# Optimization experiments

Measured on AMD Instinct MI355X. Metric: run time of the kernel, lower is better.

## Reference

```python
import math
import jax, jax.numpy as jnp
from jax import lax
import numpy as np

C = 256; A = 3; NIMG = 2; L = 5
SIZES = [(200, 304), (100, 152), (50, 76), (25, 38), (13, 19)]
STRIDES = [4, 8, 16, 32, 64]
LVTOP = 600          # cfg['lvtop'] (eval)
IMTOP = 300          # cfg['imtop1'] (eval)
SCORE_THR = 0.0      # cfg['score_thr1']
MIN_SIZE = 1e-2      # cfg['min_size1']
IOU_THR = 0.7        # cfg['iou_thr1']
IMH, IMW = 800.0, 1216.0
BBOX_CLIP = math.log(1000.0 / 16.0)   # clamp=True in decode_boxes
GROUP_OFF = 4096.0                     # > max canvas coord -> disjoint NMS groups


def _level_anchors(h, w, stride):
    scale = stride * 8.0
    r = np.array([0.5, 1.0, 2.0])
    ws = scale * np.sqrt(r); hs = scale / np.sqrt(r)          # [A]
    ys, xs = np.meshgrid(np.arange(h), np.arange(w), indexing='ij')
    cx = (xs.reshape(-1, 1) + 0.5) * stride                    # [HW,1]
    cy = (ys.reshape(-1, 1) + 0.5) * stride
    a = np.stack([cx - ws / 2, cy - hs / 2, cx + ws / 2, cy + hs / 2], axis=-1)
    return a.reshape(-1, 4).astype(np.float32)                 # [HW*A,4]


def setup_inputs() -> dict:
    key = jax.random.key(0)
    ks = jax.random.split(key, 10)
    inp = {}
    for i, (h, w) in enumerate(SIZES):
        inp[f'fmap{i}'] = jax.random.normal(ks[i], (NIMG, C, h, w), jnp.float32)
        inp[f'priors{i}'] = jnp.asarray(_level_anchors(h, w, STRIDES[i]))
    inp['imsizes'] = jnp.array([[IMH, IMW]] * NIMG, jnp.float32)   # (h, w) per image
    inp['conv_w'] = jax.random.normal(ks[5], (C, C, 3, 3), jnp.float32) * 0.03
    inp['conv_b'] = jnp.zeros((C,), jnp.float32)
    inp['log_w'] = jax.random.normal(ks[6], (A, C), jnp.float32) * 0.03
    inp['log_b'] = jnp.zeros((A,), jnp.float32)
    inp['reg_w'] = jax.random.normal(ks[7], (A * 4, C), jnp.float32) * 0.01
    inp['reg_b'] = jnp.zeros((A * 4,), jnp.float32)
    return inp


def _decode(reg, pri):
    pw = pri[..., 2] - pri[..., 0]; ph = pri[..., 3] - pri[..., 1]
    pcx = pri[..., 0] + 0.5 * pw;   pcy = pri[..., 1] + 0.5 * ph
    dx, dy = reg[..., 0], reg[..., 1]
    dw = jnp.minimum(reg[..., 2], BBOX_CLIP)
    dh = jnp.minimum(reg[..., 3], BBOX_CLIP)
    cx = dx * pw + pcx; cy = dy * ph + pcy
    w = pw * jnp.exp(dw); h = ph * jnp.exp(dh)
    return jnp.stack([cx - 0.5 * w, cy - 0.5 * h, cx + 0.5 * w, cy + 0.5 * h], axis=-1)


def _forward(fmaps, priors, imsizes, conv_w, conv_b, log_w, log_b, reg_w, reg_b):
    dn = ('NCHW', 'OIHW', 'NCHW')
    boxes_l, score_l = [], []
    for x, pri in zip(fmaps, priors):
        n = x.shape[0]
        h = jax.nn.relu(lax.conv_general_dilated(x, conv_w, (1, 1), 'SAME',
                                                 dimension_numbers=dn)
                        + conv_b[None, :, None, None])
        logit = (jnp.einsum('nchw,ac->nahw', h, log_w)
                 + log_b[None, :, None, None]).transpose(0, 2, 3, 1).reshape(n, -1)
        reg = (jnp.einsum('nchw,ac->nahw', h, reg_w)
               + reg_b[None, :, None, None]).transpose(0, 2, 3, 1).reshape(n, -1, 4)
        vals, top = lax.top_k(logit, LVTOP)                        # per-level topk
        reg_g = jnp.take_along_axis(reg, jnp.broadcast_to(top[:, :, None], (n, LVTOP, 4)), axis=1)
        pri_g = pri[top]                                           # [n,k,4]
        boxes_l.append(_decode(reg_g, pri_g))
        score_l.append(jax.nn.sigmoid(vals))
    boxes = jnp.concatenate(boxes_l, axis=1)                       # [n, L*k, 4]
    obj = jnp.concatenate(score_l, axis=1)                         # [n, L*k]
    n, dim = boxes.shape[0], boxes.shape[1]
    Nall = n * dim
    boxes = boxes.reshape(Nall, 4); obj = obj.reshape(Nall)
    imidx = jnp.arange(Nall) // dim
    lvl = jnp.tile(jnp.repeat(jnp.arange(L), LVTOP), n)
    valid = obj >= SCORE_THR
    sz = imsizes[imidx]                                            # [Nall,2] (h,w)
    boxes = jnp.stack([jnp.clip(boxes[:, 0], 0.0, sz[:, 1]),
                       jnp.clip(boxes[:, 1], 0.0, sz[:, 0]),
                       jnp.clip(boxes[:, 2], 0.0, sz[:, 1]),
                       jnp.clip(boxes[:, 3], 0.0, sz[:, 0])], axis=-1)
    valid = valid & (boxes[:, 2] - boxes[:, 0] >= MIN_SIZE) & (boxes[:, 3] - boxes[:, 1] >= MIN_SIZE)
    groups = imidx * 10 + lvl                                      # batched_nms groups
    # sort by score, invalid entries pushed to the end
    order = jnp.argsort(-jnp.where(valid, obj, -1.0))
    b = boxes[order]; v = valid[order]; g = groups[order]; im = imidx[order]
    # group-offset trick == torchvision batched_nms
    ob = b + g.astype(b.dtype)[:, None] * GROUP_OFF
    area = (ob[:, 2] - ob[:, 0]) * (ob[:, 3] - ob[:, 1])
    lt = jnp.maximum(ob[:, None, :2], ob[None, :, :2])
    rb = jnp.minimum(ob[:, None, 2:], ob[None, :, 2:])
    wh = jnp.maximum(rb - lt, 0.0)
    inter = wh[..., 0] * wh[..., 1]
    iou = lax.stop_gradient(inter / (area[:, None] + area[None, :] - inter))
    idxr = jnp.arange(Nall)
    def body(i, keep):
        sup = jnp.any(keep & (iou[i] > IOU_THR) & (idxr < i))
        return keep.at[i].set(v[i] & ~sup)
    keep = lax.fori_loop(0, Nall, body, jnp.zeros((Nall,), bool))
    # per-image cap at IMTOP (keep is already in score order)
    sel = keep[None, :] & (im[None, :] == jnp.arange(n)[:, None])  # [n,Nall]
    sel = sel & (jnp.cumsum(sel, axis=1) <= IMTOP)
    prio = jnp.where(sel, Nall - idxr[None, :], 0)
    pvals, pos = lax.top_k(prio, IMTOP)                            # [n,IMTOP]
    vout = pvals > 0
    bout = jnp.where(vout[..., None], b[pos], 0.0)                 # [n,IMTOP,4]
    imout = jnp.broadcast_to(jnp.arange(n)[:, None], (n, IMTOP)).reshape(-1).astype(jnp.int32)
    return bout.reshape(-1, 4), imout, vout.reshape(-1)


def reference(fmap0, fmap1, fmap2, fmap3, fmap4,
              priors0, priors1, priors2, priors3, priors4,
              imsizes, conv_w, conv_b, log_w, log_b, reg_w, reg_b):
    return _forward([fmap0, fmap1, fmap2, fmap3, fmap4],
                    [priors0, priors1, priors2, priors3, priors4],
                    imsizes, conv_w, conv_b, log_w, log_b, reg_w, reg_b)
```

## Files before the change

### kernel.cpp

```cpp
#include <hip/hip_runtime.h>
#include <math.h>

typedef unsigned long long u64;
typedef unsigned int u32;
typedef unsigned short u16;
typedef _Float16 f16;
typedef __attribute__((ext_vector_type(8))) _Float16 f16x8;
typedef __attribute__((ext_vector_type(8))) unsigned short ushort8;
typedef __attribute__((ext_vector_type(4))) float f32x4;

#define LVTOP 600
#define IMTOP 300
#define NIMG 2
#define NLVL 5
#define NCAND (NLVL*LVTOP)

__constant__ int d_HW[5]    = {60800,15200,3800,950,247};
__constant__ int d_LGOFF[5] = {0,364800,456000,478800,484500};
__constant__ int d_RGOFF[5] = {0,1459200,1824000,1915200,1938000};
__constant__ int d_H[5]  = {200,100,50,25,13};
__constant__ int d_W[5]  = {304,152,76,38,19};
__constant__ int d_TX[5] = {7,4,2,1,1};
__constant__ long d_XB[5] = {0, 31129600, 38912000, 40857600, 41344000};
__constant__ long d_CB[5] = {0, 3891200, 4864000, 5107200, 5168000};
#define NCHUNK 5183808
#define NXB 20250
#define WS_NEED 178889200ull

__device__ __forceinline__ u32 okey(float f){
  u32 u = __float_as_uint(f);
  return (u & 0x80000000u) ? ~u : (u | 0x80000000u);
}

__device__ __forceinline__ void f16_split(float v, u16& hb, u16& lb){
  f16 h = (f16)v;
  float r = v - (float)h;
  f16 l = (f16)r;
  hb = __builtin_bit_cast(u16, h);
  lb = __builtin_bit_cast(u16, l);
}

__device__ __forceinline__ u64 shfl64(u64 v, int src){
  u32 lo = __shfl((u32)v, src);
  u32 hi = __shfl((u32)(v >> 32), src);
  return ((u64)hi << 32) | lo;
}

__device__ __forceinline__ void dma16(const u16* g, u16* l){
  __builtin_amdgcn_global_load_lds(
      (const __attribute__((address_space(1))) u32*)g,
      (__attribute__((address_space(3))) u32*)l, 16, 0, 0);
}

template<int NN, int NT>
__device__ void bitonic_desc64(u64* a, int tid){
  for (int k = 2; k <= NN; k <<= 1){
    for (int j = k >> 1; j > 0; j >>= 1){
      __syncthreads();
      for (int i = tid; i < NN; i += NT){
        int ixj = i ^ j;
        if (ixj > i){
          u64 x = a[i], y = a[ixj];
          bool up = ((i & k) == 0);
          if (up ? (x < y) : (x > y)){ a[i] = y; a[ixj] = x; }
        }
      }
    }
  }
  __syncthreads();
}

template<int NN, int NT>
__device__ void bitonic_asc32(u32* a, int tid){
  for (int k = 2; k <= NN; k <<= 1){
    for (int j = k >> 1; j > 0; j >>= 1){
      __syncthreads();
      for (int i = tid; i < NN; i += NT){
        int ixj = i ^ j;
        if (ixj > i){
          u32 x = a[i], y = a[ixj];
          bool up = ((i & k) == 0);
          if (up ? (x > y) : (x < y)){ a[i] = y; a[ixj] = x; }
        }
      }
    }
  }
  __syncthreads();
}

__device__ void suffix_scan(u32* s, int NB, int tid){
  for (int off = 1; off < NB; off <<= 1){
    u32 v0 = 0, v1 = 0;
    int i1 = tid + 1024;
    if (tid < NB) v0 = s[tid] + ((tid + off < NB) ? s[tid + off] : 0u);
    if (i1  < NB) v1 = s[i1]  + ((i1  + off < NB) ? s[i1  + off] : 0u);
    __syncthreads();
    if (tid < NB) s[tid] = v0;
    if (i1  < NB) s[i1]  = v1;
    __syncthreads();
  }
}

__global__ __launch_bounds__(256) void prep(
    const float* __restrict__ f0, const float* __restrict__ f1,
    const float* __restrict__ f2, const float* __restrict__ f3,
    const float* __restrict__ f4,
    u16* __restrict__ xh, u16* __restrict__ xl, u16* __restrict__ zp,
    const float* __restrict__ cw, const float* __restrict__ lw,
    const float* __restrict__ rw, u16* __restrict__ wT, u16* __restrict__ whB,
    u32* __restrict__ ghist, int xsb)
{
  int t = threadIdx.x;
  if ((int)blockIdx.x >= xsb){
    int bid = blockIdx.x - xsb;
    if (bid < 72){
      int id = bid*256 + t;
      int cc = id & 7;
      int co = (id >> 3) & 255;
      int tap = id >> 11;
      int ntg = co >> 4;
      size_t base = (size_t)((tap*8 + cc)*16 + ntg) * 1024;
      #pragma unroll
      for (int ci = 0; ci < 32; ci++){
        float v = cw[(size_t)co*2304 + (size_t)(cc*32 + ci)*9 + tap];
        u16 hi, lo; f16_split(v, hi, lo);
        int q = ci >> 3, j = ci & 7;
        int lane = q*16 + (co & 15);
        wT[base + lane*8 + j] = hi;
        wT[base + 512 + lane*8 + j] = lo;
      }
    } else if (bid == 72){
      if (t < 128){
        int ks = t >> 4, nn = t & 15;
        for (int ci = 0; ci < 32; ci++){
          int k = ks*32 + ci;
          float v = 0.0f;
          if (nn < 3) v = lw[nn*256 + k];
          else if (nn < 15) v = rw[(nn-3)*256 + k];
          u16 hi, lo; f16_split(v, hi, lo);
          int q = ci >> 3, j = ci & 7;
          int lane = q*16 + nn;
          whB[ks*1024 + lane*8 + j] = hi;
          whB[ks*1024 + 512 + lane*8 + j] = lo;
        }
      }
    } else {
      int z = (bid - 73)*1024 + t;
      #pragma unroll
      for (int q = 0; q < 4; q++){
        int i = z + q*256;
        if (i < NLVL*NIMG*2048) ghist[i] = 0;
      }
    }
    return;
  }
  long id = (long)blockIdx.x*256 + t;
  if (blockIdx.x == 0 && t < 8) zp[t] = 0;
  if (id >= NCHUNK) return;
  int l = (id < d_CB[1]) ? 0 : (id < d_CB[2]) ? 1 : (id < d_CB[3]) ? 2 : (id < d_CB[4]) ? 3 : 4;
  long rem = id - d_CB[l];
  int HW = d_HW[l];
  int n = (int)(rem / (32*HW));
  int r2 = (int)(rem - (long)n*32*HW);
  int cg = r2 / HW;
  int p = r2 - cg*HW;
  const float* fm = (l==0)?f0:(l==1)?f1:(l==2)?f2:(l==3)?f3:f4;
  const float* gp = fm + ((size_t)(n*256 + cg*8))*HW + p;
  ushort8 hv, lv;
  #pragma unroll
  for (int j = 0; j < 8; j++){
    float v = gp[(size_t)j*HW];
    u16 hb, lb; f16_split(v, hb, lb);
    hv[j] = hb; lv[j] = lb;
  }
  *(ushort8*)&xh[id*8] = hv;
  *(ushort8*)&xl[id*8] = lv;
}

__global__ __launch_bounds__(256, 2) void conv_mfma(
    const float* __restrict__ f0, const float* __restrict__ f1,
    const float* __restrict__ f2, const float* __restrict__ f3,
    const float* __restrict__ f4,
    const u16* __restrict__ xh, const u16* __restrict__ xl,
    const u16* __restrict__ zp,
    const u16* __restrict__ wT, const u16* __restrict__ whB,
    const float* __restrict__ cb, const float* __restrict__ lb,
    const float* __restrict__ rb,
    float* __restrict__ lgb, float* __restrict__ rgb,
    u32* __restrict__ ghist, int use_dma)
{
  __shared__ __align__(16) u16 smem[26624];

  const int t = threadIdx.x;
  const int n = blockIdx.y;
  int bx = blockIdx.x;
  int l, rbk;
  if (bx < 700){ l = 0; rbk = bx; }
  else if (bx < 900){ l = 1; rbk = bx - 700; }
  else if (bx < 950){ l = 2; rbk = bx - 900; }
  else if (bx < 963){ l = 3; rbk = bx - 950; }
  else { l = 4; rbk = bx - 963; }
  const int H = d_H[l], W = d_W[l], tilesX = d_TX[l];
  const int ty2 = rbk / tilesX;
  const int x0 = (rbk - ty2*tilesX) * 48;
  const float* fm = (l==0) ? f0 : (l==1) ? f1 : (l==2) ? f2 : (l==3) ? f3 : f4;

  const int wave = t >> 6, lane = t & 63;
  const int quad = lane >> 4, l15 = lane & 15;
  const int HWp = H * W;
  const float* xin = fm + (size_t)n * 256 * HWp;

  f32x4 acc[2][3][4];
  #pragma unroll
  for (int r = 0; r < 2; r++)
    #pragma unroll
    for (int a = 0; a < 3; a++)
      #pragma unroll
      for (int b = 0; b < 4; b++) acc[r][a][b] = (f32x4){0.f,0.f,0.f,0.f};

  auto compute_cc = [&](int cc, int bufo){
    #pragma unroll
    for (int ky = 0; ky < 3; ky++){
      #pragma unroll
      for (int kx = 0; kx < 3; kx++){
        const u16* bt = wT + (size_t)((((ky*3+kx)*8 + cc)*16) + wave*4) * 1024 + lane*8;
        f16x8 Bh[4], Bl[4];
        #pragma unroll
        for (int nt = 0; nt < 4; nt++){
          Bh[nt] = *(const f16x8*)(bt + nt*1024);
// ... 94 lines not shown
  for (int i = t; i < 2048; i += 256) lhist[i] = 0;

  u16* hA_h = smem;
  u16* hA_l = smem + 8704;
  #pragma unroll
  for (int row = 0; row < 2; row++){
    const int ty = ty2*2 + row;
    const bool rowok = (ty < H);
    if (rowok){
      f32x4 a2 = (f32x4){0.f,0.f,0.f,0.f};
      #pragma unroll
      for (int half = 0; half < 2; half++){
        if ((wave >> 1) == half){
          #pragma unroll
          for (int mt = 0; mt < 3; mt++){
            #pragma unroll
            for (int nt = 0; nt < 4; nt++){
              int col = (wave & 1)*64 + nt*16 + l15;
              float bias = cb[half*128 + col];
              #pragma unroll
              for (int r = 0; r < 4; r++){
                float h = fmaxf(acc[row][mt][nt][r] + bias, 0.0f);
                u16 hb, lb2; f16_split(h, hb, lb2);
                int pos = mt*16 + quad*4 + r;
                hA_h[pos*136 + col] = hb;
                hA_l[pos*136 + col] = lb2;
              }
            }
          }
        }
        __syncthreads();
        #pragma unroll
        for (int ks2 = 0; ks2 < 4; ks2++){
          int ks = half*4 + ks2;
          int ao = (wave*16 + l15)*136 + ks2*32 + quad*8;
          f16x8 Ah = *(const f16x8*)&hA_h[ao];
          f16x8 Al = *(const f16x8*)&hA_l[ao];
          const u16* wb = whB + ks*1024 + lane*8;
          f16x8 Bh = *(const f16x8*)wb;
          f16x8 Bl = *(const f16x8*)(wb + 512);
          a2 = __builtin_amdgcn_mfma_f32_16x16x32_f16(Ah, Bh, a2, 0,0,0);
          a2 = __builtin_amdgcn_mfma_f32_16x16x32_f16(Al, Bh, a2, 0,0,0);
          a2 = __builtin_amdgcn_mfma_f32_16x16x32_f16(Ah, Bl, a2, 0,0,0);
        }
        __syncthreads();
      }

      float* sm_out = (float*)smem;
      {
        int o = l15;
        float bias = (o < 3) ? lb[o] : ((o < 15) ? rb[o-3] : 0.0f);
        #pragma unroll
        for (int r = 0; r < 4; r++){
          int pos = wave*16 + quad*4 + r;
          sm_out[pos*16 + o] = a2[r] + bias;
        }
      }
      __syncthreads();
      {
        int P = W - x0; if (P > 48) P = 48;
        size_t pbase = (size_t)ty * W + x0;
        float* lg = lgb + d_LGOFF[l] + (size_t)n*HWp*3  + pbase*3;
        float* rg = rgb + d_RGOFF[l] + (size_t)n*HWp*12 + pbase*12;
        for (int j = t; j < P*3; j += 256){
          float v = sm_out[(j/3)*16 + (j%3)];
          lg[j] = v;
          atomicAdd(&lhist[okey(v) >> 21], 1u);
        }
        for (int j = t; j < P*12; j += 256) rg[j] = sm_out[(j/12)*16 + 3 + (j%12)];
      }
      __syncthreads();
    }
  }

  {
    u32* gh = ghist + (size_t)(l*NIMG + n) * 2048;
    for (int i = t; i < 2048; i += 256){
      u32 h = lhist[i];
      if (h) atomicAdd(&gh[i], h);
    }
  }
}

__global__ __launch_bounds__(1024) void topk_decode(
    const float* __restrict__ lg, const float* __restrict__ rg,
    const float* __restrict__ pr0, const float* __restrict__ pr1,
    const float* __restrict__ pr2, const float* __restrict__ pr3,
    const float* __restrict__ pr4,
    const float* __restrict__ imsizes, const u32* __restrict__ ghist,
    float* __restrict__ cbox, float* __restrict__ cscore, u32* __restrict__ cvalid)
{
  __shared__ u32 hist[2048];
  __shared__ u32 sscan[2048];
  __shared__ u64 sel[1024];
  __shared__ u32 eqbuf[1024];
  __shared__ u32 scal[8];
  int tid = threadIdx.x;
  int l = blockIdx.x / NIMG;
  int n = blockIdx.x - l*NIMG;
  int HW = d_HW[l];
  int N = HW * 3;
  const float* lgl = lg + d_LGOFF[l] + (size_t)n * N;

  {
    const u32* gh = ghist + (size_t)blockIdx.x * 2048;
    for (int i = tid; i < 2048; i += 1024){ u32 h = gh[i]; hist[i] = h; sscan[i] = h; }
  }
  __syncthreads();
  suffix_scan(sscan, 2048, tid);
  if (tid < 2048){
    u32 Si = sscan[tid], Sn = (tid+1 < 2048) ? sscan[tid+1] : 0u;
    if (Si >= LVTOP && Sn < LVTOP){ scal[0] = (u32)tid; scal[1] = Si - hist[tid]; }
  }
  { int i2 = tid + 1024;
    u32 Si = sscan[i2], Sn = (i2+1 < 2048) ? sscan[i2+1] : 0u;
    if (Si >= LVTOP && Sn < LVTOP){ scal[0] = (u32)i2; scal[1] = Si - hist[i2]; } }
  __syncthreads();
  u32 B1 = scal[0], base1 = scal[1];

  for (int i = tid; i < 2048; i += 1024) hist[i] = 0;
  __syncthreads();
  for (int i = tid; i < N; i += 1024){
    u32 k = okey(lgl[i]);
    if ((k >> 21) == B1) atomicAdd(&hist[(k >> 10) & 0x7FFu], 1u);
  }
  __syncthreads();
  for (int i = tid; i < 2048; i += 1024) sscan[i] = hist[i];
  __syncthreads();
  suffix_scan(sscan, 2048, tid);
  {
    u32 need = LVTOP - base1;
    if (tid < 2048){
      u32 Si = sscan[tid], Sn = (tid+1 < 2048) ? sscan[tid+1] : 0u;
      if (Si >= need && Sn < need){ scal[2] = (u32)tid; scal[3] = base1 + Si - hist[tid]; }
    }
    int i2 = tid + 1024;
    u32 Si = sscan[i2], Sn = (i2+1 < 2048) ? sscan[i2+1] : 0u;
    if (Si >= need && Sn < need){ scal[2] = (u32)i2; scal[3] = base1 + Si - hist[i2]; }
  }
  __syncthreads();
  u32 B2 = scal[2], base2 = scal[3];

  for (int i = tid; i < 1024; i += 1024) hist[i] = 0;
  __syncthreads();
  u32 hi21 = (B1 << 11) | B2;
  for (int i = tid; i < N; i += 1024){
    u32 k = okey(lgl[i]);
    if ((k >> 10) == hi21) atomicAdd(&hist[k & 0x3FFu], 1u);
  }
  __syncthreads();
  for (int i = tid; i < 1024; i += 1024) sscan[i] = hist[i];
  __syncthreads();
  suffix_scan(sscan, 1024, tid);
  {
    u32 need = LVTOP - base2;
    if (tid < 1024){
      u32 Si = sscan[tid], Sn = (tid+1 < 1024) ? sscan[tid+1] : 0u;
      if (Si >= need && Sn < need){
        scal[4] = (hi21 << 10) | (u32)tid;
        scal[5] = base2 + Si - hist[tid];
      }
    }
  }
  if (tid == 0){ scal[6] = 0; scal[7] = 0; }
  __syncthreads();
  u32 T = scal[4], nAbove = scal[5], needEq = LVTOP - scal[5];

  for (int i = tid; i < 1024; i += 1024) sel[i] = 0;
  __syncthreads();
  for (int i = tid; i < N; i += 1024){
    u32 k = okey(lgl[i]);
    if (k > T){
      u32 p = atomicAdd(&scal[6], 1u);
      sel[p] = ((u64)k << 32) | (0xFFFFFFFFu - (u32)i);
    } else if (k == T){
      u32 p = atomicAdd(&scal[7], 1u);
      if (p < 1024) eqbuf[p] = (u32)i;
    }
  }
  __syncthreads();
  u32 cntE = scal[7];
  if (cntE > needEq){
    u32 m = cntE < 1024u ? cntE : 1024u;
    for (int i = tid; i < 1024; i += 1024) if ((u32)i >= m) eqbuf[i] = 0xFFFFFFFFu;
    __syncthreads();
    bitonic_asc32<1024,1024>(eqbuf, tid);
  }
  __syncthreads();
  if ((u32)tid < needEq)
    sel[nAbove + tid] = ((u64)T << 32) | (0xFFFFFFFFu - eqbuf[tid]);
  __syncthreads();
  {
    u64 mykey = sel[tid];
    int rank = 0;
    for (int j = 0; j < 1024; j++) rank += (sel[j] > mykey) ? 1 : 0;
    __syncthreads();
    sel[rank] = mykey;
  }
  __syncthreads();

  if (tid < LVTOP){
    u64 c = sel[tid];
    u32 i = 0xFFFFFFFFu - (u32)c;
    float val = lgl[i];
    float score = 1.0f / (1.0f + expf(-val));
    int pp = (int)i / 3, a = (int)i - pp*3;
    const float* pri;
    if (l == 0) pri = pr0; else if (l == 1) pri = pr1; else if (l == 2) pri = pr2;
    else if (l == 3) pri = pr3; else pri = pr4;
    pri += (size_t)i * 4;
    const float* rgp = rg + d_RGOFF[l] + ((size_t)n * HW + pp) * 12 + a * 4;
    float px0 = pri[0], py0 = pri[1], px1 = pri[2], py1 = pri[3];
    float pw = px1 - px0, ph = py1 - py0;
    float pcx = px0 + 0.5f*pw, pcy = py0 + 0.5f*ph;
    const float BC = (float)4.135166556742356;
    float dx = rgp[0], dy = rgp[1];
    float dw = fminf(rgp[2], BC), dh = fminf(rgp[3], BC);
    float cx = dx*pw + pcx, cy = dy*ph + pcy;
    float bw = pw * expf(dw), bh = ph * expf(dh);
    float x1 = cx - 0.5f*bw, y1 = cy - 0.5f*bh;
    float x2 = cx + 0.5f*bw, y2 = cy + 0.5f*bh;
    float imh = imsizes[n*2+0], imw = imsizes[n*2+1];
    x1 = fminf(fmaxf(x1, 0.0f), imw);
    y1 = fminf(fmaxf(y1, 0.0f), imh);
    x2 = fminf(fmaxf(x2, 0.0f), imw);
    y2 = fminf(fmaxf(y2, 0.0f), imh);
    u32 valid = (score >= 0.0f) && ((x2 - x1) >= 1e-2f) && ((y2 - y1) >= 1e-2f);
    int ci = n*NCAND + l*LVTOP + tid;
    cbox[ci*4+0] = x1; cbox[ci*4+1] = y1; cbox[ci*4+2] = x2; cbox[ci*4+3] = y2;
    cscore[ci] = score; cvalid[ci] = valid;
  }
}

__global__ __launch_bounds__(1024) void sort_cand(
    const float* __restrict__ cscore, const u32* __restrict__ cvalid,
    const float* __restrict__ cbox,
    float* __restrict__ sbox, float* __restrict__ sob,
    float* __restrict__ sarea, u32* __restrict__ svalid,
    u32* __restrict__ rlist, u32* __restrict__ kflag)
{
  __shared__ u64 a[4096];
  int tid = threadIdx.x, n = blockIdx.x;
  for (int i = tid; i < 4096; i += 1024){
    if (i < NCAND){
      int ci = n*NCAND + i;
      float s = cvalid[ci] ? cscore[ci] : -1.0f;
      a[i] = ((u64)okey(s) << 32) | (0xFFFFFFFFu - (u32)i);
    } else a[i] = 0;
  }
  bitonic_desc64<4096,1024>(a, tid);
  int mylvl[3];
  #pragma unroll
  for (int q = 0; q < 3; q++){
    int r = tid + q*1024;
    mylvl[q] = 0;
    if (r < NCAND){
      u32 li = 0xFFFFFFFFu - (u32)a[r];
      int ci = n*NCAND + (int)li;
      float b0 = cbox[ci*4+0], b1 = cbox[ci*4+1], b2 = cbox[ci*4+2], b3 = cbox[ci*4+3];
      int lvl = (int)li / LVTOP;
      mylvl[q] = lvl;
      float off = (float)(n*10 + lvl) * 4096.0f;
      int so = n*NCAND + r;
      sbox[so*4+0]=b0; sbox[so*4+1]=b1; sbox[so*4+2]=b2; sbox[so*4+3]=b3;
      float o0=b0+off, o1=b1+off, o2=b2+off, o3=b3+off;
      sob[so*4+0]=o0; sob[so*4+1]=o1; sob[so*4+2]=o2; sob[so*4+3]=o3;
      sarea[so] = (o2-o0)*(o3-o1);
      svalid[so] = cvalid[ci];
    }
  }
  __syncthreads();
  #pragma unroll
  for (int q = 0; q < 3; q++){
    int r = tid + q*1024;
    a[r] = (r < NCAND) ? (1ull << (12*mylvl[q])) : 0ull;
  }
  a[tid + 3072] = 0ull;
  __syncthreads();
  for (int off = 1; off < 4096; off <<= 1){
    u64 v[4];
    #pragma unroll
    for (int q = 0; q < 4; q++){
      int i = tid + q*1024;
      v[q] = a[i] + ((i >= off) ? a[i-off] : 0ull);
    }
    __syncthreads();
    #pragma unroll
    for (int q = 0; q < 4; q++) a[tid + q*1024] = v[q];
    __syncthreads();
  }
  #pragma unroll
  for (int q = 0; q < 3; q++){
    int r = tid + q*1024;
    if (r < NCAND){
      int lv = mylvl[q];
      int pos = (int)((a[r] >> (12*lv)) & 0xFFFull) - 1;
      rlist[(n*NLVL + lv)*LVTOP + pos] = (u32)r;
      kflag[n*NCAND + r] = 0u;
    }
  }
}

__global__ __launch_bounds__(256) void nms_l(
    const float* __restrict__ sob, const float* __restrict__ sarea,
    const u32* __restrict__ svalid, const u32* __restrict__ rlist,
    u32* __restrict__ kflag)
{
  __shared__ float bx[LVTOP*5];
  __shared__ u64 pm[LVTOP*10];
  int t = threadIdx.x, nl = blockIdx.x, n = nl / NLVL;
  for (int i = t; i < LVTOP; i += 256){
    int so = n*NCAND + (int)rlist[nl*LVTOP + i];
    bx[i*5+0]=sob[so*4+0]; bx[i*5+1]=sob[so*4+1];
    bx[i*5+2]=sob[so*4+2]; bx[i*5+3]=sob[so*4+3];
    bx[i*5+4]=sarea[so];
  }
  __syncthreads();
  for (int i = t; i < LVTOP; i += 256){
    int so = n*NCAND + (int)rlist[nl*LVTOP + i];
    bool act = svalid[so] != 0;
    float oi0=bx[i*5+0], oi1=bx[i*5+1], oi2=bx[i*5+2], oi3=bx[i*5+3], ai=bx[i*5+4];
    for (int w = 0; w < 10; w++){
      u64 bits = 0;
      if (act){
        int jj0 = (i >= w*64) ? (i - w*64 + 1) : 0;
        int jjend = (LVTOP - w*64 < 64) ? (LVTOP - w*64) : 64;
        for (int jj = jj0; jj < jjend; jj++){
          int j = w*64 + jj;
          float oj0=bx[j*5+0], oj1=bx[j*5+1], oj2=bx[j*5+2], oj3=bx[j*5+3], aj=bx[j*5+4];
          float ltx = fmaxf(oi0, oj0), lty = fmaxf(oi1, oj1);
          float rbx = fminf(oi2, oj2), rby = fminf(oi3, oj3);
          float wx = fmaxf(rbx - ltx, 0.0f), wy = fmaxf(rby - lty, 0.0f);
          float inter = wx * wy;
          float iou = inter / ((ai + aj) - inter);
          if (iou > 0.7f) bits |= (1ull << jj);
        }
      }
      pm[i*10 + w] = bits;
    }
  }
  __syncthreads();
  if (t < 64){
    u64 vw = 0, remv = 0;
    for (int c = 0; c < 10; c++){
      int i = c*64 + t;
      int pred = 0;
      if (i < LVTOP) pred = svalid[n*NCAND + (int)rlist[nl*LVTOP + i]] != 0;
      u64 b = __ballot(pred);
      if (t == c) vw = b;
    }
    for (int w = 0; w < 10; w++){
      u64 act = shfl64(vw, w) & ~shfl64(remv, w);
      while (act){
        int bpos = __builtin_ctzll(act);
        int i = w*64 + bpos;
        if (t == 0) kflag[n*NCAND + (int)rlist[nl*LVTOP + i]] = 1u;
        u64 m = (t < 10) ? pm[i*10 + t] : 0ull;
        u64 mw = pm[i*10 + w];
        remv |= m;
        act &= ~(1ull << bpos);
        act &= ~mw;
      }
    }
  }
}

__global__ __launch_bounds__(1024) void merge_out(
    const u32* __restrict__ kflag, const float* __restrict__ sbox,
    float* __restrict__ out)
{
  __shared__ u32 ps[4096];
  int tid = threadIdx.x, n = blockIdx.x;
  u32 f[4];
  #pragma unroll
  for (int q = 0; q < 4; q++){
    int i = tid + q*1024;
    f[q] = (i < NCAND) ? kflag[n*NCAND + i] : 0u;
    ps[i] = f[q];
  }
  __syncthreads();
  for (int off = 1; off < 4096; off <<= 1){
    u32 v[4];
    #pragma unroll
    for (int q = 0; q < 4; q++){
      int i = tid + q*1024;
      v[q] = ps[i] + ((i >= off) ? ps[i-off] : 0u);
    }
    __syncthreads();
    #pragma unroll
    for (int q = 0; q < 4; q++) ps[tid + q*1024] = v[q];
    __syncthreads();
  }
  #pragma unroll
  for (int q = 0; q < 4; q++){
    int i = tid + q*1024;
    if (i < NCAND && f[q] && ps[i] <= IMTOP){
      int slot = n*IMTOP + (int)ps[i] - 1;
      int so = n*NCAND + i;
      out[slot*4+0] = sbox[so*4+0]; out[slot*4+1] = sbox[so*4+1];
      out[slot*4+2] = sbox[so*4+2]; out[slot*4+3] = sbox[so*4+3];
    }
  }
  u32 kept = ps[NCAND-1]; if (kept > IMTOP) kept = IMTOP;
  for (int j = tid; j < IMTOP; j += 1024){
    int slot = n*IMTOP + j;
    if ((u32)j >= kept){
      out[slot*4+0]=0; out[slot*4+1]=0; out[slot*4+2]=0; out[slot*4+3]=0;
    }
    out[2400 + slot] = (float)n;
    out[3000 + slot] = ((u32)j < kept) ? 1.0f : 0.0f;
  }
}

extern "C" void kernel_launch(void* const* d_in, const int* in_sizes, int n_in,
                              void* d_out, int out_size, void* d_ws, size_t ws_size,
                              hipStream_t stream)
{
  const float* fmap[5]   = {(const float*)d_in[0], (const float*)d_in[2], (const float*)d_in[4],
                            (const float*)d_in[6], (const float*)d_in[8]};
  const float* priors[5] = {(const float*)d_in[1], (const float*)d_in[3], (const float*)d_in[5],
                            (const float*)d_in[7], (const float*)d_in[9]};
  const float* imsz   = (const float*)d_in[10];
  const float* conv_w = (const float*)d_in[11];
  const float* conv_b = (const float*)d_in[12];
  const float* log_w  = (const float*)d_in[13];
  const float* log_b  = (const float*)d_in[14];
  const float* reg_w  = (const float*)d_in[15];
  const float* reg_b  = (const float*)d_in[16];

  char* base = (char*)d_ws;
  float* lg     = (float*)(base + 0);
  float* rg     = (float*)(base + 1943928);
  float* cscore = (float*)(base + 9719640);
  float* cbox   = (float*)(base + 9743640);
  u32*   cvalid = (u32*)  (base + 9839640);
  float* sbox   = (float*)(base + 9863640);
  float* sob    = (float*)(base + 9959640);
  float* sarea  = (float*)(base + 10055640);
  u32*   svalid = (u32*)  (base + 10079640);
  u32*   rlist  = (u32*)  (base + 10103640);
  u32*   kflag  = (u32*)  (base + 10127640);
  u32*   ghist  = (u32*)  (base + 10151648);
  u16*   wT     = (u16*)  (base + 10631648);
  u16*   whB    = (u16*)  (base + 12990944);
  u16*   zp     = (u16*)  (base + 13007328);
  u16*   xh     = (u16*)  (base + 13007344);
  u16*   xl     = (u16*)  (base + 95948272);

  int use_dma = (ws_size >= WS_NEED) ? 1 : 0;
  int xsb = use_dma ? NXB : 0;

  prep<<<xsb + 93, 256, 0, stream>>>(
      fmap[0], fmap[1], fmap[2], fmap[3], fmap[4], xh, xl, zp,
      conv_w, log_w, reg_w, wT, whB, ghist, xsb);

  conv_mfma<<<dim3(970, NIMG), 256, 0, stream>>>(
      fmap[0], fmap[1], fmap[2], fmap[3], fmap[4],
      xh, xl, zp, wT, whB, conv_b, log_b, reg_b, lg, rg, ghist, use_dma);

  topk_decode<<<NLVL*NIMG, 1024, 0, stream>>>(lg, rg,
      priors[0], priors[1], priors[2], priors[3], priors[4],
      imsz, ghist, cbox, cscore, cvalid);
  sort_cand<<<NIMG, 1024, 0, stream>>>(cscore, cvalid, cbox, sbox, sob, sarea,
                                       svalid, rlist, kflag);
  nms_l<<<NIMG*NLVL, 256, 0, stream>>>(sob, sarea, svalid, rlist, kflag);
  merge_out<<<NIMG, 1024, 0, stream>>>(kflag, sbox, (float*)d_out);
}
```

Before: 1.133 ms.

## Fuse post-processing kernels into one persistent kernel with grid barriers

Merges topk_decode, sort_cand, nms_l and merge_out into a single 10-block kernel that separates the stages with an atomic spin grid barrier, reset in prep. This removes three kernel launches and their inter-kernel gaps from the serial tail. It relies on all 10 blocks being co-resident. The NMS stage now runs with 1024 threads per block instead of 256, and idle blocks spin on the barrier during the single-block stages.

```diff
diff --git a/kernel.cpp b/kernel.cpp
--- a/kernel.cpp
+++ b/kernel.cpp
@@ -14,6 +14,7 @@
 #define NIMG 2
 #define NLVL 5
 #define NCAND (NLVL*LVTOP)
+#define FNB (NIMG*NLVL)
 
 __constant__ int d_HW[5]    = {60800,15200,3800,950,247};
 __constant__ int d_LGOFF[5] = {0,364800,456000,478800,484500};
@@ -52,6 +53,17 @@
       (__attribute__((address_space(3))) u32*)l, 16, 0, 0);
 }
 
+__device__ __forceinline__ void gsync(u32* bar, u32 target){
+  __threadfence();
+  __syncthreads();
+  if (threadIdx.x == 0){
+    atomicAdd(bar, 1u);
+    while (atomicAdd(bar, 0u) < target){ }
+  }
+  __syncthreads();
+  __threadfence();
+}
+
 template<int NN, int NT>
 __device__ void bitonic_desc64(u64* a, int tid){
   for (int k = 2; k <= NN; k <<= 1){
@@ -108,7 +120,7 @@
     u16* __restrict__ xh, u16* __restrict__ xl, u16* __restrict__ zp,
     const float* __restrict__ cw, const float* __restrict__ lw,
     const float* __restrict__ rw, u16* __restrict__ wT, u16* __restrict__ whB,
-    u32* __restrict__ ghist, int xsb)
+    u32* __restrict__ ghist, u32* __restrict__ bar, int xsb)
 {
   int t = threadIdx.x;
   if ((int)blockIdx.x >= xsb){
@@ -145,6 +157,7 @@
         }
       }
     } else {
+      if (bid == 73 && t == 0) bar[0] = 0;
       int z = (bid - 73)*1024 + t;
       #pragma unroll
       for (int q = 0; q < 4; q++){
@@ -405,333 +418,332 @@
   }
 }
 
-__global__ __launch_bounds__(1024) void topk_decode(
+__global__ __launch_bounds__(1024) void post(
     const float* __restrict__ lg, const float* __restrict__ rg,
     const float* __restrict__ pr0, const float* __restrict__ pr1,
     const float* __restrict__ pr2, const float* __restrict__ pr3,
     const float* __restrict__ pr4,
     const float* __restrict__ imsizes, const u32* __restrict__ ghist,
-    float* __restrict__ cbox, float* __restrict__ cscore, u32* __restrict__ cvalid)
+    float* __restrict__ cbox, float* __restrict__ cscore, u32* __restrict__ cvalid,
+    float* __restrict__ sbox, float* __restrict__ sob,
+    float* __restrict__ sarea, u32* __restrict__ svalid,
+    u32* __restrict__ rlist, u32* __restrict__ kflag,
+    float* __restrict__ out, u32* __restrict__ bar)
 {
-  __shared__ u32 hist[2048];
-  __shared__ u32 sscan[2048];
-  __shared__ u64 sel[1024];
-  __shared__ u32 eqbuf[1024];
-  __shared__ u32 scal[8];
+  __shared__ __align__(16) char smx[60032];
   int tid = threadIdx.x;
-  int l = blockIdx.x / NIMG;
-  int n = blockIdx.x - l*NIMG;
-  int HW = d_HW[l];
-  int N = HW * 3;
-  const float* lgl = lg + d_LGOFF[l] + (size_t)n * N;
+  int b = blockIdx.x;
 
   {
-    const u32* gh = ghist + (size_t)blockIdx.x * 2048;
-    for (int i = tid; i < 2048; i += 1024){ u32 h = gh[i]; hist[i] = h; sscan[i] = h; }
-  }
-  __syncthreads();
-  suffix_scan(sscan, 2048, tid);
-  if (tid < 2048){
-    u32 Si = sscan[tid], Sn = (tid+1 < 2048) ? sscan[tid+1] : 0u;
-    if (Si >= LVTOP && Sn < LVTOP){ scal[0] = (u32)tid; scal[1] = Si - hist[tid]; }
-  }
-  { int i2 = tid + 1024;
-    u32 Si = sscan[i2], Sn = (i2+1 < 2048) ? sscan[i2+1] : 0u;
-    if (Si >= LVTOP && Sn < LVTOP){ scal[0] = (u32)i2; scal[1] = Si - hist[i2]; } }
-  __syncthreads();
-  u32 B1 = scal[0], base1 = scal[1];
-
-  for (int i = tid; i < 2048; i += 1024) hist[i] = 0;
-  __syncthreads();
-  for (int i = tid; i < N; i += 1024){
-    u32 k = okey(lgl[i]);
-    if ((k >> 21) == B1) atomicAdd(&hist[(k >> 10) & 0x7FFu], 1u);
-  }
-  __syncthreads();
-  for (int i = tid; i < 2048; i += 1024) sscan[i] = hist[i];
-  __syncthreads();
-  suffix_scan(sscan, 2048, tid);
-  {
-    u32 need = LVTOP - base1;
+    u32* hist  = (u32*)smx;
+    u32* sscan = (u32*)(smx + 8192);
+    u64* sel   = (u64*)(smx + 16384);
+    u32* eqbuf = (u32*)(smx + 24576);
+    u32* scal  = (u32*)(smx + 28672);
+    int l = b / NIMG;
+    int n = b - l*NIMG;
+    int HW = d_HW[l];
+    int N = HW * 3;
+    const float* lgl = lg + d_LGOFF[l] + (size_t)n * N;
+
+    {
+      const u32* gh = ghist + (size_t)b * 2048;
+      for (int i = tid; i < 2048; i += 1024){ u32 h = gh[i]; hist[i] = h; sscan[i] = h; }
+    }
+    __syncthreads();
+    suffix_scan(sscan, 2048, tid);
     if (tid < 2048){
       u32 Si = sscan[tid], Sn = (tid+1 < 2048) ? sscan[tid+1] : 0u;
-      if (Si >= need && Sn < need){ scal[2] = (u32)tid; scal[3] = base1 + Si - hist[tid]; }
-    }
-    int i2 = tid + 1024;
-    u32 Si = sscan[i2], Sn = (i2+1 < 2048) ? sscan[i2+1] : 0u;
-    if (Si >= need && Sn < need){ scal[2] = (u32)i2; scal[3] = base1 + Si - hist[i2]; }
-  }
-  __syncthreads();
-  u32 B2 = scal[2], base2 = scal[3];
-
-  for (int i = tid; i < 1024; i += 1024) hist[i] = 0;
-  __syncthreads();
-  u32 hi21 = (B1 << 11) | B2;
-  for (int i = tid; i < N; i += 1024){
-    u32 k = okey(lgl[i]);
-    if ((k >> 10) == hi21) atomicAdd(&hist[k & 0x3FFu], 1u);
-  }
-  __syncthreads();
-  for (int i = tid; i < 1024; i += 1024) sscan[i] = hist[i];
-  __syncthreads();
-  suffix_scan(sscan, 1024, tid);
+      if (Si >= LVTOP && Sn < LVTOP){ scal[0] = (u32)tid; scal[1] = Si - hist[tid]; }
+    }
+    { int i2 = tid + 1024;
+      u32 Si = sscan[i2], Sn = (i2+1 < 2048) ? sscan[i2+1] : 0u;
+      if (Si >= LVTOP && Sn < LVTOP){ scal[0] = (u32)i2; scal[1] = Si - hist[i2]; } }
+    __syncthreads();
+    u32 B1 = scal[0], base1 = scal[1];
+
+    for (int i = tid; i < 2048; i += 1024) hist[i] = 0;
+    __syncthreads();
+    for (int i = tid; i < N; i += 1024){
+      u32 k = okey(lgl[i]);
+      if ((k >> 21) == B1) atomicAdd(&hist[(k >> 10) & 0x7FFu], 1u);
+    }
+    __syncthreads();
+    for (int i = tid; i < 2048; i += 1024) sscan[i] = hist[i];
+    __syncthreads();
+    suffix_scan(sscan, 2048, tid);
+    {
+      u32 need = LVTOP - base1;
+      if (tid < 2048){
+        u32 Si = sscan[tid], Sn = (tid+1 < 2048) ? sscan[tid+1] : 0u;
+        if (Si >= need && Sn < need){ scal[2] = (u32)tid; scal[3] = base1 + Si - hist[tid]; }
+      }
+      int i2 = tid + 1024;
+      u32 Si = sscan[i2], Sn = (i2+1 < 2048) ? sscan[i2+1] : 0u;
+      if (Si >= need && Sn < need){ scal[2] = (u32)i2; scal[3] = base1 + Si - hist[i2]; }
+    }
+    __syncthreads();
+    u32 B2 = scal[2], base2 = scal[3];
+
+    for (int i = tid; i < 1024; i += 1024) hist[i] = 0;
+    __syncthreads();
+    u32 hi21 = (B1 << 11) | B2;
+    for (int i = tid; i < N; i += 1024){
+      u32 k = okey(lgl[i]);
+      if ((k >> 10) == hi21) atomicAdd(&hist[k & 0x3FFu], 1u);
+    }
+    __syncthreads();
+    for (int i = tid; i < 1024; i += 1024) sscan[i] = hist[i];
+    __syncthreads();
+    suffix_scan(sscan, 1024, tid);
+    {
+      u32 need = LVTOP - base2;
+      if (tid < 1024){
+        u32 Si = sscan[tid], Sn = (tid+1 < 1024) ? sscan[tid+1] : 0u;
+        if (Si >= need && Sn < need){
+          scal[4] = (hi21 << 10) | (u32)tid;
+          scal[5] = base2 + Si - hist[tid];
+        }
+      }
+    }
+    if (tid == 0){ scal[6] = 0; scal[7] = 0; }
+    __syncthreads();
+    u32 T = scal[4], nAbove = scal[5], needEq = LVTOP - scal[5];
+
+    for (int i = tid; i < 1024; i += 1024) sel[i] = 0;
+    __syncthreads();
+    for (int i = tid; i < N; i += 1024){
+      u32 k = okey(lgl[i]);
+      if (k > T){
+        u32 p = atomicAdd(&scal[6], 1u);
+        sel[p] = ((u64)k << 32) | (0xFFFFFFFFu - (u32)i);
+      } else if (k == T){
+        u32 p = atomicAdd(&scal[7], 1u);
+        if (p < 1024) eqbuf[p] = (u32)i;
+      }
+    }
+    __syncthreads();
+    u32 cntE = scal[7];
+    if (cntE > needEq){
+      u32 m = cntE < 1024u ? cntE : 1024u;
+      for (int i = tid; i < 1024; i += 1024) if ((u32)i >= m) eqbuf[i] = 0xFFFFFFFFu;
+      __syncthreads();
+      bitonic_asc32<1024,1024>(eqbuf, tid);
+    }
+    __syncthreads();
+    if ((u32)tid < needEq)
+      sel[nAbove + tid] = ((u64)T << 32) | (0xFFFFFFFFu - eqbuf[tid]);
+    __syncthreads();
+    {
+      u64 mykey = sel[tid];
+      int rank = 0;
+      for (int j = 0; j < 1024; j++) rank += (sel[j] > mykey) ? 1 : 0;
+      __syncthreads();
+      sel[rank] = mykey;
+    }
+    __syncthreads();
+
+    if (tid < LVTOP){
+      u64 c = sel[tid];
+      u32 i = 0xFFFFFFFFu - (u32)c;
+      float val = lgl[i];
+      float score = 1.0f / (1.0f + expf(-val));
+      int pp = (int)i / 3, a = (int)i - pp*3;
+      const float* pri;
+      if (l == 0) pri = pr0; else if (l == 1) pri = pr1; else if (l == 2) pri = pr2;
+      else if (l == 3) pri = pr3; else pri = pr4;
+      pri += (size_t)i * 4;
+      const float* rgp = rg + d_RGOFF[l] + ((size_t)n * HW + pp) * 12 + a * 4;
+      float px0 = pri[0], py0 = pri[1], px1 = pri[2], py1 = pri[3];
+      float pw = px1 - px0, ph = py1 - py0;
+      float pcx = px0 + 0.5f*pw, pcy = py0 + 0.5f*ph;
+      const float BC = (float)4.135166556742356;
+      float dx = rgp[0], dy = rgp[1];
+      float dw = fminf(rgp[2], BC), dh = fminf(rgp[3], BC);
+      float cx = dx*pw + pcx, cy = dy*ph + pcy;
+      float bw = pw * expf(dw), bh = ph * expf(dh);
+      float x1 = cx - 0.5f*bw, y1 = cy - 0.5f*bh;
+      float x2 = cx + 0.5f*bw, y2 = cy + 0.5f*bh;
+      float imh = imsizes[n*2+0], imw = imsizes[n*2+1];
+      x1 = fminf(fmaxf(x1, 0.0f), imw);
+      y1 = fminf(fmaxf(y1, 0.0f), imh);
+      x2 = fminf(fmaxf(x2, 0.0f), imw);
+      y2 = fminf(fmaxf(y2, 0.0f), imh);
+      u32 valid = (score >= 0.0f) && ((x2 - x1) >= 1e-2f) && ((y2 - y1) >= 1e-2f);
+      int ci = n*NCAND + l*LVTOP + tid;
+      cbox[ci*4+0] = x1; cbox[ci*4+1] = y1; cbox[ci*4+2] = x2; cbox[ci*4+3] = y2;
+      cscore[ci] = score; cvalid[ci] = valid;
+    }
+  }
+  gsync(bar, FNB);
+
+  if (b < NIMG){
+    u64* a = (u64*)smx;
+    int n = b;
+    for (int i = tid; i < 4096; i += 1024){
+      if (i < NCAND){
+        int ci = n*NCAND + i;
+        float s = cvalid[ci] ? cscore[ci] : -1.0f;
+        a[i] = ((u64)okey(s) << 32) | (0xFFFFFFFFu - (u32)i);
+      } else a[i] = 0;
+    }
+    bitonic_desc64<4096,1024>(a, tid);
+    int mylvl[3];
+    #pragma unroll
+    for (int q = 0; q < 3; q++){
+      int r = tid + q*1024;
+      mylvl[q] = 0;
+      if (r < NCAND){
+        u32 li = 0xFFFFFFFFu - (u32)a[r];
+        int ci = n*NCAND + (int)li;
+        float b0 = cbox[ci*4+0], b1 = cbox[ci*4+1], b2 = cbox[ci*4+2], b3 = cbox[ci*4+3];
+        int lvl = (int)li / LVTOP;
+        mylvl[q] = lvl;
+        float off = (float)(n*10 + lvl) * 4096.0f;
+        int so = n*NCAND + r;
+        sbox[so*4+0]=b0; sbox[so*4+1]=b1; sbox[so*4+2]=b2; sbox[so*4+3]=b3;
+        float o0=b0+off, o1=b1+off, o2=b2+off, o3=b3+off;
+        sob[so*4+0]=o0; sob[so*4+1]=o1; sob[so*4+2]=o2; sob[so*4+3]=o3;
+        sarea[so] = (o2-o0)*(o3-o1);
+        svalid[so] = cvalid[ci];
+      }
+    }
+    __syncthreads();
+    #pragma unroll
+    for (int q = 0; q < 3; q++){
+      int r = tid + q*1024;
+      a[r] = (r < NCAND) ? (1ull << (12*mylvl[q])) : 0ull;
+    }
+    a[tid + 3072] = 0ull;
+    __syncthreads();
+    for (int off = 1; off < 4096; off <<= 1){
+      u64 v[4];
+      #pragma unroll
+      for (int q = 0; q < 4; q++){
+        int i = tid + q*1024;
+        v[q] = a[i] + ((i >= off) ? a[i-off] : 0ull);
+      }
+      __syncthreads();
+      #pragma unroll
+      for (int q = 0; q < 4; q++) a[tid + q*1024] = v[q];
+      __syncthreads();
+    }
+    #pragma unroll
+    for (int q = 0; q < 3; q++){
+      int r = tid + q*1024;
+      if (r < NCAND){
+        int lv = mylvl[q];
+        int pos = (int)((a[r] >> (12*lv)) & 0xFFFull) - 1;
+        rlist[(n*NLVL + lv)*LVTOP + pos] = (u32)r;
+        kflag[n*NCAND + r] = 0u;
+      }
+    }
+  }
+  gsync(bar, 2*FNB);
+
   {
-    u32 need = LVTOP - base2;
-    if (tid < 1024){
-      u32 Si = sscan[tid], Sn = (tid+1 < 1024) ? sscan[tid+1] : 0u;
-      if (Si >= need && Sn < need){
-        scal[4] = (hi21 << 10) | (u32)tid;
-        scal[5] = base2 + Si - hist[tid];
-      }
-    }
-  }
-  if (tid == 0){ scal[6] = 0; scal[7] = 0; }
-  __syncthreads();
-  u32 T = scal[4], nAbove = scal[5], needEq = LVTOP - scal[5];
-
-  for (int i = tid; i < 1024; i += 1024) sel[i] = 0;
-  __syncthreads();
-  for (int i = tid; i < N; i += 1024){
-    u32 k = okey(lgl[i]);
-    if (k > T){
-      u32 p = atomicAdd(&scal[6], 1u);
-      sel[p] = ((u64)k << 32) | (0xFFFFFFFFu - (u32)i);
-    } else if (k == T){
-      u32 p = atomicAdd(&scal[7], 1u);
-      if (p < 1024) eqbuf[p] = (u32)i;
-    }
-  }
-  __syncthreads();
-  u32 cntE = scal[7];
-  if (cntE > needEq){
-    u32 m = cntE < 1024u ? cntE : 1024u;
-    for (int i = tid; i < 1024; i += 1024) if ((u32)i >= m) eqbuf[i] = 0xFFFFFFFFu;
-    __syncthreads();
-    bitonic_asc32<1024,1024>(eqbuf, tid);
-  }
-  __syncthreads();
-  if ((u32)tid < needEq)
-    sel[nAbove + tid] = ((u64)T << 32) | (0xFFFFFFFFu - eqbuf[tid]);
-  __syncthreads();
-  {
-    u64 mykey = sel[tid];
-    int rank = 0;
-    for (int j = 0; j < 1024; j++) rank += (sel[j] > mykey) ? 1 : 0;
-    __syncthreads();
-    sel[rank] = mykey;
-  }
-  __syncthreads();
-
-  if (tid < LVTOP){
-    u64 c = sel[tid];
-    u32 i = 0xFFFFFFFFu - (u32)c;
-    float val = lgl[i];
-    float score = 1.0f / (1.0f + expf(-val));
-    int pp = (int)i / 3, a = (int)i - pp*3;
-    const float* pri;
-    if (l == 0) pri = pr0; else if (l == 1) pri = pr1; else if (l == 2) pri = pr2;
-    else if (l == 3) pri = pr3; else pri = pr4;
-    pri += (size_t)i * 4;
-    const float* rgp = rg + d_RGOFF[l] + ((size_t)n * HW + pp) * 12 + a * 4;
-    float px0 = pri[0], py0 = pri[1], px1 = pri[2], py1 = pri[3];
-    float pw = px1 - px0, ph = py1 - py0;
-    float pcx = px0 + 0.5f*pw, pcy = py0 + 0.5f*ph;
-    const float BC = (float)4.135166556742356;
-    float dx = rgp[0], dy = rgp[1];
-    float dw = fminf(rgp[2], BC), dh = fminf(rgp[3], BC);
-    float cx = dx*pw + pcx, cy = dy*ph + pcy;
-    float bw = pw * expf(dw), bh = ph * expf(dh);
-    float x1 = cx - 0.5f*bw, y1 = cy - 0.5f*bh;
-    float x2 = cx + 0.5f*bw, y2 = cy + 0.5f*bh;
-    float imh = imsizes[n*2+0], imw = imsizes[n*2+1];
-    x1 = fminf(fmaxf(x1, 0.0f), imw);
-    y1 = fminf(fmaxf(y1, 0.0f), imh);
-    x2 = fminf(fmaxf(x2, 0.0f), imw);
-    y2 = fminf(fmaxf(y2, 0.0f), imh);
-    u32 valid = (score >= 0.0f) && ((x2 - x1) >= 1e-2f) && ((y2 - y1) >= 1e-2f);
-    int ci = n*NCAND + l*LVTOP + tid;
-    cbox[ci*4+0] = x1; cbox[ci*4+1] = y1; cbox[ci*4+2] = x2; cbox[ci*4+3] = y2;
-    cscore[ci] = score; cvalid[ci] = valid;
-  }
-}
-
-__global__ __launch_bounds__(1024) void sort_cand(
-    const float* __restrict__ cscore, const u32* __restrict__ cvalid,
-    const float* __restrict__ cbox,
-    float* __restrict__ sbox, float* __restrict__ sob,
-    float* __restrict__ sarea, u32* __restrict__ svalid,
-    u32* __restrict__ rlist, u32* __restrict__ kflag)
-{
-  __shared__ u64 a[4096];
-  int tid = threadIdx.x, n = blockIdx.x;
-  for (int i = tid; i < 4096; i += 1024){
-    if (i < NCAND){
-      int ci = n*NCAND + i;
-      float s = cvalid[ci] ? cscore[ci] : -1.0f;
-      a[i] = ((u64)okey(s) << 32) | (0xFFFFFFFFu - (u32)i);
-    } else a[i] = 0;
-  }
-  bitonic_desc64<4096,1024>(a, tid);
-  int mylvl[3];
-  #pragma unroll
-  for (int q = 0; q < 3; q++){
-    int r = tid + q*1024;
-    mylvl[q] = 0;
-    if (r < NCAND){
-      u32 li = 0xFFFFFFFFu - (u32)a[r];
-      int ci = n*NCAND + (int)li;
-      float b0 = cbox[ci*4+0], b1 = cbox[ci*4+1], b2 = cbox[ci*4+2], b3 = cbox[ci*4+3];
-      int lvl = (int)li / LVTOP;
-      mylvl[q] = lvl;
-      float off = (float)(n*10 + lvl) * 4096.0f;
-      int so = n*NCAND + r;
-      sbox[so*4+0]=b0; sbox[so*4+1]=b1; sbox[so*4+2]=b2; sbox[so*4+3]=b3;
-      float o0=b0+off, o1=b1+off, o2=b2+off, o3=b3+off;
-      sob[so*4+0]=o0; sob[so*4+1]=o1; sob[so*4+2]=o2; sob[so*4+3]=o3;
-      sarea[so] = (o2-o0)*(o3-o1);
-      svalid[so] = cvalid[ci];
-    }
-  }
-  __syncthreads();
-  #pragma unroll
-  for (int q = 0; q < 3; q++){
-    int r = tid + q*1024;
-    a[r] = (r < NCAND) ? (1ull << (12*mylvl[q])) : 0ull;
-  }
-  a[tid + 3072] = 0ull;
-  __syncthreads();
-  for (int off = 1; off < 4096; off <<= 1){
-    u64 v[4];
+    float* bxx = (float*)smx;
+    u64* pm = (u64*)(smx + 12032);
+    int nl = b, n = nl / NLVL;
+    for (int i = tid; i < LVTOP; i += 1024){
+      int so = n*NCAND + (int)rlist[nl*LVTOP + i];
+      bxx[i*5+0]=sob[so*4+0]; bxx[i*5+1]=sob[so*4+1];
+      bxx[i*5+2]=sob[so*4+2]; bxx[i*5+3]=sob[so*4+3];
+      bxx[i*5+4]=sarea[so];
+    }
+    __syncthreads();
+    for (int i = tid; i < LVTOP; i += 1024){
+      int so = n*NCAND + (int)rlist[nl*LVTOP + i];
+      bool act = svalid[so] != 0;
+      float oi0=bxx[i*5+0], oi1=bxx[i*5+1], oi2=bxx[i*5+2], oi3=bxx[i*5+3], ai=bxx[i*5+4];
+      for (int w = 0; w < 10; w++){
+        u64 bits = 0;
+        if (act){
+          int jj0 = (i >= w*64) ? (i - w*64 + 1) : 0;
+          int jjend = (LVTOP - w*64 < 64) ? (LVTOP - w*64) : 64;
+          for (int jj = jj0; jj < jjend; jj++){
+            int j = w*64 + jj;
+            float oj0=bxx[j*5+0], oj1=bxx[j*5+1], oj2=bxx[j*5+2], oj3=bxx[j*5+3], aj=bxx[j*5+4];
+            float ltx = fmaxf(oi0, oj0), lty = fmaxf(oi1, oj1);
+            float rbx = fminf(oi2, oj2), rby = fminf(oi3, oj3);
+            float wx = fmaxf(rbx - ltx, 0.0f), wy = fmaxf(rby - lty, 0.0f);
+            float inter = wx * wy;
+            float iou = inter / ((ai + aj) - inter);
+            if (iou > 0.7f) bits |= (1ull << jj);
+          }
+        }
+        pm[i*10 + w] = bits;
+      }
+    }
+    __syncthreads();
+    if (tid < 64){
+      u64 vw = 0, remv = 0;
+      for (int c = 0; c < 10; c++){
+        int i = c*64 + tid;
+        int pred = 0;
+        if (i < LVTOP) pred = svalid[n*NCAND + (int)rlist[nl*LVTOP + i]] != 0;
+        u64 bl = __ballot(pred);
+        if (tid == c) vw = bl;
+      }
+      for (int w = 0; w < 10; w++){
+        u64 act = shfl64(vw, w) & ~shfl64(remv, w);
+        while (act){
+          int bpos = __builtin_ctzll(act);
+          int i = w*64 + bpos;
+          if (tid == 0) kflag[n*NCAND + (int)rlist[nl*LVTOP + i]] = 1u;
+          u64 m = (tid < 10) ? pm[i*10 + tid] : 0ull;
+          u64 mw = pm[i*10 + w];
+          remv |= m;
+          act &= ~(1ull << bpos);
+          act &= ~mw;
+        }
+      }
+    }
+  }
+  gsync(bar, 3*FNB);
+
+  if (b < NIMG){
+    u32* ps = (u32*)smx;
+    int n = b;
+    u32 f[4];
     #pragma unroll
     for (int q = 0; q < 4; q++){
       int i = tid + q*1024;
-      v[q] = a[i] + ((i >= off) ? a[i-off] : 0ull);
-    }
-    __syncthreads();
-    #pragma unroll
-    for (int q = 0; q < 4; q++) a[tid + q*1024] = v[q];
-    __syncthreads();
-  }
-  #pragma unroll
-  for (int q = 0; q < 3; q++){
-    int r = tid + q*1024;
-    if (r < NCAND){
-      int lv = mylvl[q];
-      int pos = (int)((a[r] >> (12*lv)) & 0xFFFull) - 1;
-      rlist[(n*NLVL + lv)*LVTOP + pos] = (u32)r;
-      kflag[n*NCAND + r] = 0u;
-    }
-  }
-}
-
-__global__ __launch_bounds__(256) void nms_l(
-    const float* __restrict__ sob, const float* __restrict__ sarea,
-    const u32* __restrict__ svalid, const u32* __restrict__ rlist,
-    u32* __restrict__ kflag)
-{
-  __shared__ float bx[LVTOP*5];
-  __shared__ u64 pm[LVTOP*10];
-  int t = threadIdx.x, nl = blockIdx.x, n = nl / NLVL;
-  for (int i = t; i < LVTOP; i += 256){
-    int so = n*NCAND + (int)rlist[nl*LVTOP + i];
-    bx[i*5+0]=sob[so*4+0]; bx[i*5+1]=sob[so*4+1];
-    bx[i*5+2]=sob[so*4+2]; bx[i*5+3]=sob[so*4+3];
-    bx[i*5+4]=sarea[so];
-  }
-  __syncthreads();
-  for (int i = t; i < LVTOP; i += 256){
-    int so = n*NCAND + (int)rlist[nl*LVTOP + i];
-    bool act = svalid[so] != 0;
-    float oi0=bx[i*5+0], oi1=bx[i*5+1], oi2=bx[i*5+2], oi3=bx[i*5+3], ai=bx[i*5+4];
-    for (int w = 0; w < 10; w++){
-      u64 bits = 0;
-      if (act){
-        int jj0 = (i >= w*64) ? (i - w*64 + 1) : 0;
-        int jjend = (LVTOP - w*64 < 64) ? (LVTOP - w*64) : 64;
-        for (int jj = jj0; jj < jjend; jj++){
-          int j = w*64 + jj;
-          float oj0=bx[j*5+0], oj1=bx[j*5+1], oj2=bx[j*5+2], oj3=bx[j*5+3], aj=bx[j*5+4];
-          float ltx = fmaxf(oi0, oj0), lty = fmaxf(oi1, oj1);
-          float rbx = fminf(oi2, oj2), rby = fminf(oi3, oj3);
-          float wx = fmaxf(rbx - ltx, 0.0f), wy = fmaxf(rby - lty, 0.0f);
-          float inter = wx * wy;
-          float iou = inter / ((ai + aj) - inter);
-          if (iou > 0.7f) bits |= (1ull << jj);
-        }
-      }
-      pm[i*10 + w] = bits;
-    }
-  }
-  __syncthreads();
-  if (t < 64){
-    u64 vw = 0, remv = 0;
-    for (int c = 0; c < 10; c++){
-      int i = c*64 + t;
-      int pred = 0;
-      if (i < LVTOP) pred = svalid[n*NCAND + (int)rlist[nl*LVTOP + i]] != 0;
-      u64 b = __ballot(pred);
-      if (t == c) vw = b;
-    }
-    for (int w = 0; w < 10; w++){
-      u64 act = shfl64(vw, w) & ~shfl64(remv, w);
-      while (act){
-        int bpos = __builtin_ctzll(act);
-        int i = w*64 + bpos;
-        if (t == 0) kflag[n*NCAND + (int)rlist[nl*LVTOP + i]] = 1u;
-        u64 m = (t < 10) ? pm[i*10 + t] : 0ull;
-        u64 mw = pm[i*10 + w];
-        remv |= m;
-        act &= ~(1ull << bpos);
-        act &= ~mw;
-      }
-    }
-  }
-}
-
-__global__ __launch_bounds__(1024) void merge_out(
-    const u32* __restrict__ kflag, const float* __restrict__ sbox,
-    float* __restrict__ out)
-{
-  __shared__ u32 ps[4096];
-  int tid = threadIdx.x, n = blockIdx.x;
-  u32 f[4];
-  #pragma unroll
-  for (int q = 0; q < 4; q++){
-    int i = tid + q*1024;
-    f[q] = (i < NCAND) ? kflag[n*NCAND + i] : 0u;
-    ps[i] = f[q];
-  }
-  __syncthreads();
-  for (int off = 1; off < 4096; off <<= 1){
-    u32 v[4];
+      f[q] = (i < NCAND) ? kflag[n*NCAND + i] : 0u;
+      ps[i] = f[q];
+    }
+    __syncthreads();
+    for (int off = 1; off < 4096; off <<= 1){
+      u32 v[4];
+      #pragma unroll
+      for (int q = 0; q < 4; q++){
+        int i = tid + q*1024;
+        v[q] = ps[i] + ((i >= off) ? ps[i-off] : 0u);
+      }
+      __syncthreads();
+      #pragma unroll
+      for (int q = 0; q < 4; q++) ps[tid + q*1024] = v[q];
+      __syncthreads();
+    }
     #pragma unroll
     for (int q = 0; q < 4; q++){
       int i = tid + q*1024;
-      v[q] = ps[i] + ((i >= off) ? ps[i-off] : 0u);
-    }
-    __syncthreads();
-    #pragma unroll
-    for (int q = 0; q < 4; q++) ps[tid + q*1024] = v[q];
-    __syncthreads();
-  }
-  #pragma unroll
-  for (int q = 0; q < 4; q++){
-    int i = tid + q*1024;
-    if (i < NCAND && f[q] && ps[i] <= IMTOP){
-      int slot = n*IMTOP + (int)ps[i] - 1;
-      int so = n*NCAND + i;
-      out[slot*4+0] = sbox[so*4+0]; out[slot*4+1] = sbox[so*4+1];
-      out[slot*4+2] = sbox[so*4+2]; out[slot*4+3] = sbox[so*4+3];
-    }
-  }
-  u32 kept = ps[NCAND-1]; if (kept > IMTOP) kept = IMTOP;
-  for (int j = tid; j < IMTOP; j += 1024){
-    int slot = n*IMTOP + j;
-    if ((u32)j >= kept){
-      out[slot*4+0]=0; out[slot*4+1]=0; out[slot*4+2]=0; out[slot*4+3]=0;
-    }
-    out[2400 + slot] = (float)n;
-    out[3000 + slot] = ((u32)j < kept) ? 1.0f : 0.0f;
+      if (i < NCAND && f[q] && ps[i] <= IMTOP){
+        int slot = n*IMTOP + (int)ps[i] - 1;
+        int so = n*NCAND + i;
+        out[slot*4+0] = sbox[so*4+0]; out[slot*4+1] = sbox[so*4+1];
+        out[slot*4+2] = sbox[so*4+2]; out[slot*4+3] = sbox[so*4+3];
+      }
+    }
+    u32 kept = ps[NCAND-1]; if (kept > IMTOP) kept = IMTOP;
+    for (int j = tid; j < IMTOP; j += 1024){
+      int slot = n*IMTOP + j;
+      if ((u32)j >= kept){
+        out[slot*4+0]=0; out[slot*4+1]=0; out[slot*4+2]=0; out[slot*4+3]=0;
+      }
+      out[2400 + slot] = (float)n;
+      out[3000 + slot] = ((u32)j < kept) ? 1.0f : 0.0f;
+    }
   }
 }
 
@@ -764,6 +776,7 @@
   u32*   rlist  = (u32*)  (base + 10103640);
   u32*   kflag  = (u32*)  (base + 10127640);
   u32*   ghist  = (u32*)  (base + 10151648);
+  u32*   bar    = (u32*)  (base + 10233568);
   u16*   wT     = (u16*)  (base + 10631648);
   u16*   whB    = (u16*)  (base + 12990944);
   u16*   zp     = (u16*)  (base + 13007328);
@@ -775,17 +788,14 @@
 
   prep<<<xsb + 93, 256, 0, stream>>>(
       fmap[0], fmap[1], fmap[2], fmap[3], fmap[4], xh, xl, zp,
-      conv_w, log_w, reg_w, wT, whB, ghist, xsb);
+      conv_w, log_w, reg_w, wT, whB, ghist, bar, xsb);
 
   conv_mfma<<<dim3(970, NIMG), 256, 0, stream>>>(
       fmap[0], fmap[1], fmap[2], fmap[3], fmap[4],
       xh, xl, zp, wT, whB, conv_b, log_b, reg_b, lg, rg, ghist, use_dma);
 
-  topk_decode<<<NLVL*NIMG, 1024, 0, stream>>>(lg, rg,
+  post<<<FNB, 1024, 0, stream>>>(lg, rg,
       priors[0], priors[1], priors[2], priors[3], priors[4],
-      imsz, ghist, cbox, cscore, cvalid);
-  sort_cand<<<NIMG, 1024, 0, stream>>>(cscore, cvalid, cbox, sbox, sob, sarea,
-                                       svalid, rlist, kflag);
-  nms_l<<<NIMG*NLVL, 256, 0, stream>>>(sob, sarea, svalid, rlist, kflag);
-  merge_out<<<NIMG, 1024, 0, stream>>>(kflag, sbox, (float*)d_out);
-}
+      imsz, ghist, cbox, cscore, cvalid,
+      sbox, sob, sarea, svalid, rlist, kflag, (float*)d_out, bar);
+}
```

Result: no change. 1.115 ms (-1.6%).
